# Optimization experiments

Measured on AMD Instinct MI355X. Metric: run time of the kernel, lower is better.

The kernel has to match this reference:

```python
import jax, jax.numpy as jnp
import numpy as np

B, N, D = 4, 1024, 32      # clouds, points per cloud, feature dim
NW = 4                     # n_weights
THRESHOLD = 0.5
J = 3                      # wavelet scales (as in forward: J = 3)


def setup_inputs() -> dict:
    key = jax.random.key(0)
    k1, k2 = jax.random.split(key)
    point_clouds = jax.random.normal(k1, (B, N, D), dtype=jnp.float32)
    alphas = jax.random.uniform(k2, (NW, D), dtype=jnp.float32)
    sigma = jnp.float32(50.0)
    return {"point_clouds": point_clouds, "alphas": alphas, "sigma": sigma}


def reference(point_clouds, alphas, sigma):
    # X_nodes = pc * alpha_w for every (cloud p, weight w): [B, NW, N, D]
    X = point_clouds[:, None, :, :] * alphas[None, :, None, :]
    # compute_dist: ||xi||^2 + ||xj||^2 - 2 <xi, xj>  -> [B, NW, N, N]
    sq = jnp.sum(X * X, axis=-1)
    G = jnp.einsum('bwnd,bwmd->bwnm', X, X)
    Dm = sq[..., :, None] + sq[..., None, :] - 2.0 * G
    K = jnp.exp(-Dm / sigma)
    # threshold graph: keep kernel weight where K >= threshold (self-loops kept, K_ii = 1)
    A = (K >= THRESHOLD).astype(X.dtype)
    Wm = K * A
    deg = jnp.sum(Wm, axis=-1)  # >= 1 via self-loop
    # lazy random-walk diffusion operator P = 0.5 (I + D^{-1} W)
    P = 0.5 * (jnp.eye(N, dtype=X.dtype) + Wm / deg[..., None])
    # dyadic powers P^(2^j), j = 0..J
    powers = [P]
    for _ in range(J):
        powers.append(jnp.einsum('bwnm,bwmk->bwnk', powers[-1], powers[-1]))

    def apply(M, F):
        return jnp.einsum('bwnm,bwmd->bwnd', M, F)

    # first-order scattering |psi_j X| with psi_j = P^(2^(j)) - P^(2^(j+1))
    first = [jnp.abs(apply(powers[j] - powers[j + 1], X)) for j in range(J)]
    # second-order |psi_k |psi_j X|| for j < k
    second = [jnp.abs(apply(powers[k] - powers[k + 1], first[j]))
              for j in range(J) for k in range(j + 1, J)]
    feats = jnp.concatenate([X] + first + second, axis=-1)  # [B, NW, N, F0]
    pooled = jnp.mean(feats, axis=2)                        # mean pooling -> [B, NW, F0]
    # final view(B_pc, features * n_weights)
    return pooled.reshape(B, -1)
```

## Files before the change

kernel.cpp:

```cpp
#include <hip/hip_runtime.h>
#include <math.h>

#define NPTS 1024
#define DIM 32
#define NPAIR 16

typedef __attribute__((ext_vector_type(8))) short short8;
typedef __attribute__((ext_vector_type(4))) float f32x4;
typedef __attribute__((ext_vector_type(8))) unsigned short ushort8v;
typedef unsigned short u16;
typedef unsigned char u8;


__device__ __forceinline__ u16 bf16_rne(float v) {
    unsigned u = __float_as_uint(v);
    return (u16)((u + 0x7fffu + ((u >> 16) & 1u)) >> 16);
}
__device__ __forceinline__ float bf16_to_f32(u16 b) {
    return __uint_as_float(((unsigned)b) << 16);
}

__device__ __forceinline__ short8 unpack_w8(unsigned lo, unsigned hi) {
    short8 r;
#pragma unroll
    for (int j = 0; j < 4; j++) {
        float f0 = (float)((lo >> (8 * j)) & 0xffu);
        float f1 = (float)((hi >> (8 * j)) & 0xffu);
        r[j]     = (short)(__float_as_uint(f0) >> 16);
        r[j + 4] = (short)(__float_as_uint(f1) >> 16);
    }
    return r;
}

__global__ __launch_bounds__(256) void build_X(const float* __restrict__ pc,
                                               const float* __restrict__ alphas,
                                               float* __restrict__ X,
                                               float* __restrict__ sqX,
                                               float* __restrict__ deg,
                                               u16* __restrict__ hiT,
                                               u16* __restrict__ loT,
                                               float* __restrict__ poolP) {
    __shared__ float S[DIM][68];
    int pair = blockIdx.y, n0 = blockIdx.x * 64, tid = threadIdx.x;
    int b = pair >> 2, w = pair & 3;
    for (int e = tid; e < 512; e += 256) {
        int e4 = e * 4;
        int dn = e4 >> 5, dq = e4 & 31;
        float4 p = *(const float4*)&pc[((size_t)b * NPTS + n0 + dn) * DIM + dq];
        float4 al = *(const float4*)&alphas[w * DIM + dq];
        float4 x = make_float4(p.x * al.x, p.y * al.y, p.z * al.z, p.w * al.w);
        *(float4*)&X[((size_t)pair * NPTS + n0 + dn) * DIM + dq] = x;
        S[dq][dn] = x.x; S[dq + 1][dn] = x.y; S[dq + 2][dn] = x.z; S[dq + 3][dn] = x.w;
    }
    __syncthreads();
    if (tid < 64) {
        float s = 0.f;
#pragma unroll
        for (int d = 0; d < DIM; d++) { float v = S[d][tid]; s += v * v; }
        sqX[pair * NPTS + n0 + tid] = s;
        deg[pair * NPTS + n0 + tid] = 0.0f;
    }
    if (tid < 64) {
        int h = tid >> 5, d = tid & 31;
        float s = 0.f;
#pragma unroll
        for (int k = 0; k < 32; k++) s += S[d][h * 32 + k];
        poolP[(((size_t)0 * NPAIR + pair) * 32 + 2 * blockIdx.x + h) * 32 + d] = s;
    }
    for (int idx = tid; idx < DIM * 4; idx += 256) {
        int row = idx >> 2, nq = (idx & 3) * 16;
        ushort8v hv[2], lv[2];
#pragma unroll
        for (int i = 0; i < 16; i++) {
            float v = S[row][nq + i];
            u16 hb = bf16_rne(v);
            hv[i >> 3][i & 7] = hb;
            lv[i >> 3][i & 7] = bf16_rne(v - bf16_to_f32(hb));
        }
        int c0 = n0 + nq;
        int kt = c0 >> 5;
        int q0 = (c0 >> 3) & 3;
        int mm = row & 15;
        size_t base = ((((size_t)pair * 2 + (row >> 4)) * 32 + kt) << 9);
        *(ushort8v*)(hiT + base + (size_t)(q0 * 16 + mm) * 8)       = hv[0];
        *(ushort8v*)(hiT + base + (size_t)((q0 + 1) * 16 + mm) * 8) = hv[1];
        *(ushort8v*)(loT + base + (size_t)(q0 * 16 + mm) * 8)       = lv[0];
        *(ushort8v*)(loT + base + (size_t)((q0 + 1) * 16 + mm) * 8) = lv[1];
    }
}

__global__ __launch_bounds__(256, 4) void W_kernel(const float* __restrict__ X,
                                                   const float* __restrict__ sqX,
                                                   const float* __restrict__ sigp,
                                                   float* __restrict__ deg,
                                                   u8* __restrict__ W8) {
    int bid = blockIdx.x;
    int xcd = bid & 7, loc = bid >> 3;
    int pair = xcd * 2 + (loc & 1);
    int j0 = ((loc >> 1) & 3) * 256;
    int i0 = (loc >> 3) * 64;
    float rsig = -1.0f / (*sigp);
    const float* Xp = X + (size_t)pair * NPTS * DIM;

    __shared__ float XiT[DIM][68];
    __shared__ float XjT[DIM][68];
    __shared__ float sqjS[64];

    int tid = threadIdx.x;
    int cx = tid & 15, ry = tid >> 4;

    {
        int r = tid & 63, dgb = (tid >> 6) * 4;
#pragma unroll
        for (int p = 0; p < 2; p++) {
            int dg = dgb + p * 16;
            float4 v = *(const float4*)&Xp[(size_t)(i0 + r) * DIM + dg];
            XiT[dg][r] = v.x; XiT[dg + 1][r] = v.y; XiT[dg + 2][r] = v.z; XiT[dg + 3][r] = v.w;
        }
    }
    float sqi[4];
#pragma unroll
    for (int a = 0; a < 4; a++) sqi[a] = sqX[pair * NPTS + i0 + ry * 4 + a];

    float rs[4] = {0.f, 0.f, 0.f, 0.f};
#pragma unroll 1
    for (int jt = 0; jt < 256; jt += 64) {
        __syncthreads();
        {
            int r = tid & 63, dgb = (tid >> 6) * 4;
#pragma unroll
            for (int p = 0; p < 2; p++) {
                int dg = dgb + p * 16;
                float4 v = *(const float4*)&Xp[(size_t)(j0 + jt + r) * DIM + dg];
                XjT[dg][r] = v.x; XjT[dg + 1][r] = v.y; XjT[dg + 2][r] = v.z; XjT[dg + 3][r] = v.w;
            }
        }
        if (tid < 64) sqjS[tid] = sqX[pair * NPTS + j0 + jt + tid];
        __syncthreads();

        float dot[4][4] = {};
#pragma unroll
        for (int d = 0; d < DIM; d++) {
            float4 a = *(const float4*)&XiT[d][ry * 4];
            float4 b = *(const float4*)&XjT[d][cx * 4];
            dot[0][0] += a.x * b.x; dot[0][1] += a.x * b.y; dot[0][2] += a.x * b.z; dot[0][3] += a.x * b.w;
            dot[1][0] += a.y * b.x; dot[1][1] += a.y * b.y; dot[1][2] += a.y * b.z; dot[1][3] += a.y * b.w;
            dot[2][0] += a.z * b.x; dot[2][1] += a.z * b.y; dot[2][2] += a.z * b.z; dot[2][3] += a.z * b.w;
            dot[3][0] += a.w * b.x; dot[3][1] += a.w * b.y; dot[3][2] += a.w * b.z; dot[3][3] += a.w * b.w;
        }
#pragma unroll
        for (int a = 0; a < 4; a++) {
            int i = i0 + ry * 4 + a;
            int jb = j0 + jt + cx * 4;
            unsigned qw = 0;
#pragma unroll
            for (int bb = 0; bb < 4; bb++) {
                float Dm = sqi[a] + sqjS[cx * 4 + bb] - 2.0f * dot[a][bb];
                float K = __expf(Dm * rsig);
                float Wv = (K >= 0.5f) ? K : 0.0f;
                unsigned q = (unsigned)fmaf(Wv, 255.0f, 0.5f);
                rs[a] += (float)q;
                qw |= q << (8 * bb);
            }
            int kt = jb >> 5;
            int quad = (jb >> 3) & 3;
            int jj = jb & 7;
            size_t o = ((((size_t)pair * 64 + (i >> 4)) * 32 + kt) << 9)
                     + (size_t)(quad * 16 + (i & 15)) * 8 + jj;
            *(unsigned*)(W8 + o) = qw;
        }
    }
#pragma unroll
    for (int a = 0; a < 4; a++) {
        float s = rs[a];
        s += __shfl_xor(s, 1); s += __shfl_xor(s, 2);
        s += __shfl_xor(s, 4); s += __shfl_xor(s, 8);
        if (cx == 0) atomicAdd(&deg[pair * NPTS + i0 + ry * 4 + a], s);
    }
}

template <int DC>
__global__ __launch_bounds__(512, 4) void apply_fused(const u8* __restrict__ W8,
                                                      const u16* __restrict__ Yhi,
                                                      const u16* __restrict__ Ylo,
                                                      const float* __restrict__ deg,
                                                      const float* __restrict__ prevF,
                                                      int prevStride, int prevOff,
                                                      float* __restrict__ dstF,
                                                      int dstStride, int dstOff,
                                                      float* __restrict__ sliceF,
                                                      u16* __restrict__ hiT, u16* __restrict__ loT,
                                                      int tC0, int tCN) {
    constexpr int NT = DC / 16;
    constexpr int SP = DC + 4;
    __shared__ float S[4][32][SP];
    __shared__ float rdegS[32];
    int bid = blockIdx.x;
    int pair = (bid & 7) * 2 + ((bid >> 3) & 1);
    int r0 = (bid >> 4) * 32;
    int tid = threadIdx.x;
    int wv = tid >> 6, lane = tid & 63;
    int m = lane & 15, quad = lane >> 4;

    if (tid < 32) rdegS[tid] = 0.5f / deg[pair * NPTS + r0 + tid];

    int rt0 = (bid >> 4) * 2;
    const u8*  Wb  = W8  + ((((size_t)pair * 64 + rt0) * 32 + wv * 4) << 9) + (size_t)lane * 8;
    const u16* Ybh = Yhi + (((size_t)pair * NT * 32 + wv * 4) << 9) + (size_t)lane * 8;
    const u16* Ybl = Ylo + (((size_t)pair * NT * 32 + wv * 4) << 9) + (size_t)lane * 8;

    f32x4 acc[2][NT];
#pragma unroll
    for (int mt = 0; mt < 2; mt++)
#pragma unroll
        for (int nt = 0; nt < NT; nt++)
#pragma unroll
            for (int i = 0; i < 4; i++) acc[mt][nt][i] = 0.0f;

#pragma unroll 2
    for (int c = 0; c < 4; c++) {
        uint2 a0q = *(const uint2*)(Wb + ((size_t)c << 9));
        uint2 a1q = *(const uint2*)(Wb + ((size_t)(32 + c) << 9));
        short8 a0h = unpack_w8(a0q.x, a0q.y);
        short8 a1h = unpack_w8(a1q.x, a1q.y);
#pragma unroll
        for (int nt = 0; nt < NT; nt++) {
            short8 bh = *(const short8*)(Ybh + ((size_t)(nt * 32 + c) << 9));
            short8 bl = *(const short8*)(Ybl + ((size_t)(nt * 32 + c) << 9));
            acc[0][nt] = __builtin_amdgcn_mfma_f32_16x16x32_bf16(a0h, bh, acc[0][nt], 0, 0, 0);
            acc[0][nt] = __builtin_amdgcn_mfma_f32_16x16x32_bf16(a0h, bl, acc[0][nt], 0, 0, 0);
            acc[1][nt] = __builtin_amdgcn_mfma_f32_16x16x32_bf16(a1h, bh, acc[1][nt], 0, 0, 0);
            acc[1][nt] = __builtin_amdgcn_mfma_f32_16x16x32_bf16(a1h, bl, acc[1][nt], 0, 0, 0);
        }
    }

    if (wv < 4) {
#pragma unroll
        for (int mt = 0; mt < 2; mt++)
#pragma unroll
            for (int nt = 0; nt < NT; nt++)
#pragma unroll
                for (int i = 0; i < 4; i++)
                    S[wv][mt * 16 + quad * 4 + i][nt * 16 + m] = acc[mt][nt][i];
    }
    __syncthreads();
    if (wv >= 4) {
#pragma unroll
        for (int mt = 0; mt < 2; mt++)
#pragma unroll
            for (int nt = 0; nt < NT; nt++)
#pragma unroll
                for (int i = 0; i < 4; i++)
                    S[wv - 4][mt * 16 + quad * 4 + i][nt * 16 + m] += acc[mt][nt][i];
    }
    __syncthreads();

    constexpr int E2 = 32 * DC / 4;
    for (int e = tid; e < E2; e += 512) {
        int e4 = e * 4;
        int n = e4 / DC, d = e4 % DC;
        float4 s0 = *(const float4*)&S[0][n][d];
        float4 s1 = *(const float4*)&S[1][n][d];
        float4 s2 = *(const float4*)&S[2][n][d];
        float4 s3 = *(const float4*)&S[3][n][d];
        float4 pv = *(const float4*)&prevF[((size_t)pair * NPTS + r0 + n) * prevStride + prevOff + d];
        float r = rdegS[n];
        float4 o = make_float4(0.5f * pv.x + r * (s0.x + s1.x + s2.x + s3.x),
                               0.5f * pv.y + r * (s0.y + s1.y + s2.y + s3.y),
                               0.5f * pv.z + r * (s0.z + s1.z + s2.z + s3.z),
                               0.5f * pv.w + r * (s0.w + s1.w + s2.w + s3.w));
        *(float4*)&dstF[((size_t)pair * NPTS + r0 + n) * dstStride + dstOff + d] = o;
        if (sliceF && d >= 32 && d < 64)
            *(float4*)&sliceF[((size_t)pair * NPTS + r0 + n) * 32 + (d - 32)] = o;
        *(float4*)&S[0][n][d] = o;
    }
    __syncthreads();

    if (hiT) {
        int NFo = tCN >> 4;
        for (int e = tid; e < tCN * 4; e += 512) {
            int row = e >> 2, nq = (e & 3) * 8;
            ushort8v hv, lv;
#pragma unroll
            for (int j = 0; j < 8; j++) {
                float v = S[0][nq + j][tC0 + row];
                u16 hb = bf16_rne(v);
                hv[j] = hb;
                lv[j] = bf16_rne(v - bf16_to_f32(hb));
            }
            int c0 = r0 + nq;
            size_t o = ((((size_t)pair * NFo + (row >> 4)) * 32 + (c0 >> 5)) << 9)
                     + (size_t)((((c0 >> 3) & 3) * 16 + (row & 15))) * 8;
            *(ushort8v*)(hiT + o) = hv;
            *(ushort8v*)(loT + o) = lv;
        }
    }
}

__global__ __launch_bounds__(512, 4) void apply_fused_m0(const u8* __restrict__ W8,
                                                         const u16* __restrict__ Yhi,
                                                         const u16* __restrict__ Ylo,
                                                         const float* __restrict__ deg,
                                                         const float* __restrict__ prevF,
                                                         const float* __restrict__ A1,
                                                         const float* __restrict__ A2,
                                                         float* __restrict__ M0,
                                                         u16* __restrict__ hiT, u16* __restrict__ loT,
                                                         float* __restrict__ poolP) {
    constexpr int DC = 32, NT = 2, SP = 36;
    __shared__ float S[4][32][SP];
    __shared__ float rdegS[32];
    __shared__ float SB[96][33];
    int bid = blockIdx.x;
    int pair = (bid & 7) * 2 + ((bid >> 3) & 1);
    int r0 = (bid >> 4) * 32;
    int rt = bid >> 4;
    int tid = threadIdx.x;
    int wv = tid >> 6, lane = tid & 63;
    int m = lane & 15, quad = lane >> 4;

    if (tid < 32) rdegS[tid] = 0.5f / deg[pair * NPTS + r0 + tid];

    int rt0 = rt * 2;
    const u8*  Wb  = W8  + ((((size_t)pair * 64 + rt0) * 32 + wv * 4) << 9) + (size_t)lane * 8;
    const u16* Ybh = Yhi + (((size_t)pair * NT * 32 + wv * 4) << 9) + (size_t)lane * 8;
    const u16* Ybl = Ylo + (((size_t)pair * NT * 32 + wv * 4) << 9) + (size_t)lane * 8;

    f32x4 acc[2][NT];
#pragma unroll
    for (int mt = 0; mt < 2; mt++)
#pragma unroll
        for (int nt = 0; nt < NT; nt++)
#pragma unroll
            for (int i = 0; i < 4; i++) acc[mt][nt][i] = 0.0f;

#pragma unroll 2
    for (int c = 0; c < 4; c++) {
        uint2 a0q = *(const uint2*)(Wb + ((size_t)c << 9));
        uint2 a1q = *(const uint2*)(Wb + ((size_t)(32 + c) << 9));
        short8 a0h = unpack_w8(a0q.x, a0q.y);
        short8 a1h = unpack_w8(a1q.x, a1q.y);
#pragma unroll
        for (int nt = 0; nt < NT; nt++) {
            short8 bh = *(const short8*)(Ybh + ((size_t)(nt * 32 + c) << 9));
            short8 bl = *(const short8*)(Ybl + ((size_t)(nt * 32 + c) << 9));
            acc[0][nt] = __builtin_amdgcn_mfma_f32_16x16x32_bf16(a0h, bh, acc[0][nt], 0, 0, 0);
            acc[0][nt] = __builtin_amdgcn_mfma_f32_16x16x32_bf16(a0h, bl, acc[0][nt], 0, 0, 0);
            acc[1][nt] = __builtin_amdgcn_mfma_f32_16x16x32_bf16(a1h, bh, acc[1][nt], 0, 0, 0);
            acc[1][nt] = __builtin_amdgcn_mfma_f32_16x16x32_bf16(a1h, bl, acc[1][nt], 0, 0, 0);
        }
    }

    if (wv < 4) {
#pragma unroll
        for (int mt = 0; mt < 2; mt++)
#pragma unroll
            for (int nt = 0; nt < NT; nt++)
#pragma unroll
                for (int i = 0; i < 4; i++)
                    S[wv][mt * 16 + quad * 4 + i][nt * 16 + m] = acc[mt][nt][i];
    }
    __syncthreads();
    if (wv >= 4) {
#pragma unroll
        for (int mt = 0; mt < 2; mt++)
#pragma unroll
            for (int nt = 0; nt < NT; nt++)
#pragma unroll
                for (int i = 0; i < 4; i++)
                    S[wv - 4][mt * 16 + quad * 4 + i][nt * 16 + m] += acc[mt][nt][i];
    }
    __syncthreads();

    for (int e = tid; e < 256; e += 512) {
        int e4 = e * 4;
        int n = e4 / DC, d = e4 % DC;
        float4 s0 = *(const float4*)&S[0][n][d];
        float4 s1 = *(const float4*)&S[1][n][d];
        float4 s2 = *(const float4*)&S[2][n][d];
        float4 s3 = *(const float4*)&S[3][n][d];
        float4 pv = *(const float4*)&prevF[((size_t)pair * NPTS + r0 + n) * 32 + d];
        float r = rdegS[n];
        float4 o = make_float4(0.5f * pv.x + r * (s0.x + s1.x + s2.x + s3.x),
                               0.5f * pv.y + r * (s0.y + s1.y + s2.y + s3.y),
                               0.5f * pv.z + r * (s0.z + s1.z + s2.z + s3.z),
                               0.5f * pv.w + r * (s0.w + s1.w + s2.w + s3.w));
        *(float4*)&M0[((size_t)pair * NPTS + r0 + n) * 96 + d] = o;
        *(float4*)&S[0][n][d] = o;
    }
    __syncthreads();

    if (tid < 256) {
        int dn = tid >> 3, dq = (tid & 7) * 4;
        size_t pn = (size_t)pair * NPTS + r0 + dn;
        float4 a1 = *(const float4*)&A1[pn * 32 + dq];
        float4 a2 = *(const float4*)&A2[pn * 32 + dq];
        float4 t4 = *(const float4*)&S[0][dn][dq];
        float4 f0 = make_float4(fabsf(a1.x - a2.x), fabsf(a1.y - a2.y), fabsf(a1.z - a2.z), fabsf(a1.w - a2.w));
        float4 f1 = make_float4(fabsf(a2.x - t4.x), fabsf(a2.y - t4.y), fabsf(a2.z - t4.z), fabsf(a2.w - t4.w));
        *(float4*)&M0[pn * 96 + 32 + dq] = f0;
        *(float4*)&M0[pn * 96 + 64 + dq] = f1;
        SB[dq][dn] = t4.x; SB[dq + 1][dn] = t4.y; SB[dq + 2][dn] = t4.z; SB[dq + 3][dn] = t4.w;
        SB[32 + dq][dn] = f0.x; SB[33 + dq][dn] = f0.y; SB[34 + dq][dn] = f0.z; SB[35 + dq][dn] = f0.w;
        SB[64 + dq][dn] = f1.x; SB[65 + dq][dn] = f1.y; SB[66 + dq][dn] = f1.z; SB[67 + dq][dn] = f1.w;
    }
    __syncthreads();

    if (tid < 64) {
        int gg = tid >> 5, d = tid & 31;
        float s = 0.f;
#pragma unroll
        for (int k = 0; k < 32; k++) s += SB[32 + gg * 32 + d][k];
        poolP[(((size_t)(1 + gg) * NPAIR + pair) * 32 + rt) * 32 + d] = s;
    }

    for (int e = tid; e < 96 * 4; e += 512) {
        int row = e >> 2, nq = (e & 3) * 8;
        ushort8v hv, lv;
#pragma unroll
        for (int j = 0; j < 8; j++) {
            float v = SB[row][nq + j];
            u16 hb = bf16_rne(v);
            hv[j] = hb;
            lv[j] = bf16_rne(v - bf16_to_f32(hb));
        }
        int c0 = r0 + nq;
        size_t o = ((((size_t)pair * 6 + (row >> 4)) * 32 + (c0 >> 5)) << 9)
                 + (size_t)((((c0 >> 3) & 3) * 16 + (row & 15))) * 8;
        *(ushort8v*)(hiT + o) = hv;
        *(ushort8v*)(loT + o) = lv;
    }
}

__global__ __launch_bounds__(512, 4) void apply_fused_pool(const u8* __restrict__ W8,
                                                           const u16* __restrict__ Yhi,
                                                           const u16* __restrict__ Ylo,
                                                           const float* __restrict__ deg,
                                                           const float* __restrict__ prevF,
                                                           float* __restrict__ Z8,
                                                           const float* __restrict__ M0,
                                                           const float* __restrict__ M2p,
                                                           const float* __restrict__ M4f,
                                                           float* __restrict__ poolP) {
    constexpr int DC = 64, NT = 4, SP = 68;
    __shared__ float S[4][32][SP];
    __shared__ float rdegS[32];
    __shared__ float PP[4][2][32];
    int bid = blockIdx.x;
    int pair = (bid & 7) * 2 + ((bid >> 3) & 1);
    int r0 = (bid >> 4) * 32;
    int rt = bid >> 4;
    int tid = threadIdx.x;
    int wv = tid >> 6, lane = tid & 63;
    int m = lane & 15, quad = lane >> 4;

    if (tid < 32) rdegS[tid] = 0.5f / deg[pair * NPTS + r0 + tid];

    int rt0 = rt * 2;
    const u8*  Wb  = W8  + ((((size_t)pair * 64 + rt0) * 32 + wv * 4) << 9) + (size_t)lane * 8;
    const u16* Ybh = Yhi + (((size_t)pair * NT * 32 + wv * 4) << 9) + (size_t)lane * 8;
    const u16* Ybl = Ylo + (((size_t)pair * NT * 32 + wv * 4) << 9) + (size_t)lane * 8;

    f32x4 acc[2][NT];
#pragma unroll
    for (int mt = 0; mt < 2; mt++)
#pragma unroll
        for (int nt = 0; nt < NT; nt++)
#pragma unroll
            for (int i = 0; i < 4; i++) acc[mt][nt][i] = 0.0f;

#pragma unroll 2
    for (int c = 0; c < 4; c++) {
        uint2 a0q = *(const uint2*)(Wb + ((size_t)c << 9));
        uint2 a1q = *(const uint2*)(Wb + ((size_t)(32 + c) << 9));
        short8 a0h = unpack_w8(a0q.x, a0q.y);
        short8 a1h = unpack_w8(a1q.x, a1q.y);
#pragma unroll
        for (int nt = 0; nt < NT; nt++) {
            short8 bh = *(const short8*)(Ybh + ((size_t)(nt * 32 + c) << 9));
            short8 bl = *(const short8*)(Ybl + ((size_t)(nt * 32 + c) << 9));
            acc[0][nt] = __builtin_amdgcn_mfma_f32_16x16x32_bf16(a0h, bh, acc[0][nt], 0, 0, 0);
            acc[0][nt] = __builtin_amdgcn_mfma_f32_16x16x32_bf16(a0h, bl, acc[0][nt], 0, 0, 0);
            acc[1][nt] = __builtin_amdgcn_mfma_f32_16x16x32_bf16(a1h, bh, acc[1][nt], 0, 0, 0);
            acc[1][nt] = __builtin_amdgcn_mfma_f32_16x16x32_bf16(a1h, bl, acc[1][nt], 0, 0, 0);
        }
    }

    if (wv < 4) {
#pragma unroll
        for (int mt = 0; mt < 2; mt++)
#pragma unroll
            for (int nt = 0; nt < NT; nt++)
#pragma unroll
                for (int i = 0; i < 4; i++)
                    S[wv][mt * 16 + quad * 4 + i][nt * 16 + m] = acc[mt][nt][i];
    }
    __syncthreads();
    if (wv >= 4) {
#pragma unroll
        for (int mt = 0; mt < 2; mt++)
#pragma unroll
            for (int nt = 0; nt < NT; nt++)
#pragma unroll
                for (int i = 0; i < 4; i++)
                    S[wv - 4][mt * 16 + quad * 4 + i][nt * 16 + m] += acc[mt][nt][i];
    }
    __syncthreads();

    for (int e = tid; e < 512; e += 512) {
        int e4 = e * 4;
        int n = e4 / DC, d = e4 % DC;
        float4 s0 = *(const float4*)&S[0][n][d];
        float4 s1 = *(const float4*)&S[1][n][d];
        float4 s2 = *(const float4*)&S[2][n][d];
        float4 s3 = *(const float4*)&S[3][n][d];
        float4 pv = *(const float4*)&prevF[((size_t)pair * NPTS + r0 + n) * 64 + d];
        float r = rdegS[n];
        float4 o = make_float4(0.5f * pv.x + r * (s0.x + s1.x + s2.x + s3.x),
                               0.5f * pv.y + r * (s0.y + s1.y + s2.y + s3.y),
                               0.5f * pv.z + r * (s0.z + s1.z + s2.z + s3.z),
                               0.5f * pv.w + r * (s0.w + s1.w + s2.w + s3.w));
        *(float4*)&Z8[((size_t)pair * NPTS + r0 + n) * 64 + d] = o;
        *(float4*)&S[0][n][d] = o;
    }
    __syncthreads();

    if (tid < 256) {
        int gsel = tid >> 6, h = (tid >> 5) & 1, d = tid & 31;
        float s = 0.f;
#pragma unroll 4
        for (int k = 0; k < 16; k++) {
            int n = h * 16 + k;
            size_t pn = (size_t)pair * NPTS + r0 + n;
            float v;
            switch (gsel) {
                case 0: v = fabsf(M0[pn * 96 + d] - M4f[pn * 96 + d]); break;
                case 1: v = fabsf(M2p[pn * 32 + d] - M4f[pn * 96 + 32 + d]); break;
                case 2: v = fabsf(M4f[pn * 96 + 32 + d] - S[0][n][d]); break;
                default: v = fabsf(M4f[pn * 96 + 64 + d] - S[0][n][32 + d]); break;
            }
            s += v;
        }
        PP[gsel][h][d] = s;
    }
    __syncthreads();
    if (tid < 128) {
        int gsel = tid >> 5, d = tid & 31;
        poolP[(((size_t)(3 + gsel) * NPAIR + pair) * 32 + rt) * 32 + d] = PP[gsel][0][d] + PP[gsel][1][d];
    }
}

__global__ __launch_bounds__(256) void pool_final(const float* __restrict__ partial,
                                                  float* __restrict__ out) {
    int pair = blockIdx.x;
    int t = threadIdx.x;
    if (t < 224) {
        int g = t >> 5, d = t & 31;
        float s = 0.0f;
#pragma unroll 8
        for (int r = 0; r < 32; r++)
            s += partial[(((size_t)g * NPAIR + pair) * 32 + r) * 32 + d];
        out[(size_t)pair * 224 + t] = s * (1.0f / 1024.0f);
    }
}

extern "C" void kernel_launch(void* const* d_in, const int* in_sizes, int n_in,
                              void* d_out, int out_size, void* d_ws, size_t ws_size,
                              hipStream_t stream) {
    const float* pc     = (const float*)d_in[0];
    const float* alphas = (const float*)d_in[1];
    const float* sigp   = (const float*)d_in[2];
    float* out = (float*)d_out;
    float* ws = (float*)d_ws;

    float* X    = ws;
    float* sqX  = X + 524288;
    float* deg  = sqX + 16384;
    u8* W8 = (u8*)(deg + 16384);
    float* A1   = (float*)(W8 + 16777216);
    float* A2   = A1 + 524288;
    u16* T32a_h = (u16*)(A2 + 524288);
    u16* T32a_l = T32a_h + 524288;
    u16* T32b_h = T32a_l + 524288;
    u16* T32b_l = T32b_h + 524288;
    float* F96b = A1;
    float* M0   = (float*)(T32b_l + 524288);
    float* M2p  = M0 + 1572864;
    float* M4f  = M2p + 524288;
    float* Z8   = M4f + 1572864;
    float* F96a = Z8 + 1048576;
    float* A3   = F96a;
    u16* T96a_h = (u16*)(F96a + 1572864);
    u16* T96a_l = T96a_h + 1572864;
    u16* T96b_h = T96a_l + 1572864;
    u16* T96b_l = T96b_h + 1572864;
    u16* T64a_h = T96a_h;
    u16* T64a_l = T96a_l;
    u16* T64b_h = T96b_h;
    u16* T64b_l = T96b_l;
    float* poolP = (float*)(T96b_l + 1572864);

    dim3 b256(256), b512(512);

    build_X<<<dim3(16, NPAIR), b256, 0, stream>>>(pc, alphas, X, sqX, deg, T32a_h, T32a_l, poolP);
    W_kernel<<<dim3(1024), b256, 0, stream>>>(X, sqX, sigp, deg, W8);

    apply_fused<32><<<dim3(512), b512, 0, stream>>>(W8, T32a_h, T32a_l, deg,
                                             X, 32, 0, A1, 32, 0, nullptr, T32b_h, T32b_l, 0, 32);
    apply_fused<32><<<dim3(512), b512, 0, stream>>>(W8, T32b_h, T32b_l, deg,
                                             A1, 32, 0, A2, 32, 0, nullptr, T32a_h, T32a_l, 0, 32);
    apply_fused<32><<<dim3(512), b512, 0, stream>>>(W8, T32a_h, T32a_l, deg,
                                             A2, 32, 0, A3, 32, 0, nullptr, T32b_h, T32b_l, 0, 32);
    apply_fused_m0<<<dim3(512), b512, 0, stream>>>(W8, T32b_h, T32b_l, deg,
                                             A3, A1, A2, M0, T96a_h, T96a_l, poolP);

    apply_fused<96><<<dim3(512), b512, 0, stream>>>(W8, T96a_h, T96a_l, deg,
                                             M0, 96, 0, F96a, 96, 0, nullptr, T96b_h, T96b_l, 0, 96);
    apply_fused<96><<<dim3(512), b512, 0, stream>>>(W8, T96b_h, T96b_l, deg,
                                             F96a, 96, 0, F96b, 96, 0, M2p, T96a_h, T96a_l, 0, 96);
    apply_fused<96><<<dim3(512), b512, 0, stream>>>(W8, T96a_h, T96a_l, deg,
                                             F96b, 96, 0, F96a, 96, 0, nullptr, T96b_h, T96b_l, 0, 96);
    apply_fused<96><<<dim3(512), b512, 0, stream>>>(W8, T96b_h, T96b_l, deg,
                                             F96a, 96, 0, M4f, 96, 0, nullptr, T64a_h, T64a_l, 32, 64);

    apply_fused<64><<<dim3(512), b512, 0, stream>>>(W8, T64a_h, T64a_l, deg,
                                             M4f, 96, 32, F96a, 64, 0, nullptr, T64b_h, T64b_l, 0, 64);
    apply_fused<64><<<dim3(512), b512, 0, stream>>>(W8, T64b_h, T64b_l, deg,
                                             F96a, 64, 0, F96b, 64, 0, nullptr, T64a_h, T64a_l, 0, 64);
    apply_fused<64><<<dim3(512), b512, 0, stream>>>(W8, T64a_h, T64a_l, deg,
                                             F96b, 64, 0, F96a, 64, 0, nullptr, T64b_h, T64b_l, 0, 64);
    apply_fused_pool<<<dim3(512), b512, 0, stream>>>(W8, T64b_h, T64b_l, deg,
                                             F96a, Z8, M0, M2p, M4f, poolP);

    pool_final<<<dim3(NPAIR), b256, 0, stream>>>(poolP, out);
}
```

Before: 235.2 us.

## Retile wide apply kernels to 64-row by 32-column blocks split over column chunks

Adds apply_fused2 and apply_fused_pool2, which give each block 64 rows and one 32-column chunk of the feature matrix instead of 32 rows and all columns. The 96- and 64-column diffusion applies and the final pooling kernel now use this tiling, with more blocks for the 96-wide case. Each loaded W tile is reused across four row tiles per wave and the number of resident accumulators per thread is bounded. In exchange, the W8 matrix is re-read once per column chunk, and the pooling partial sums are split by chunk with direct writes to poolP.

Result: faster. 224.5 us (-4.6%).

```diff
diff --git a/kernel.cpp b/kernel.cpp
--- a/kernel.cpp
+++ b/kernel.cpp
@@ -297,6 +297,130 @@
     }
 }
 
+template <int DC>
+__global__ __launch_bounds__(512, 4) void apply_fused2(const u8* __restrict__ W8,
+                                                       const u16* __restrict__ Yhi,
+                                                       const u16* __restrict__ Ylo,
+                                                       const float* __restrict__ deg,
+                                                       const float* __restrict__ prevF,
+                                                       int prevStride, int prevOff,
+                                                       float* __restrict__ dstF,
+                                                       int dstStride, int dstOff,
+                                                       float* __restrict__ sliceF,
+                                                       u16* __restrict__ hiT, u16* __restrict__ loT,
+                                                       int tC0, int tCN) {
+    constexpr int NF = DC / 16;
+    constexpr int SP = 36;
+    __shared__ float S[4][64][SP];
+    __shared__ float rdegS[64];
+    int bid = blockIdx.x;
+    int pair = (bid & 7) * 2 + ((bid >> 3) & 1);
+    int rseg = (bid >> 4) & 15;
+    int ch = bid >> 8;
+    int r0 = rseg * 64;
+    int tid = threadIdx.x;
+    int wv = tid >> 6, lane = tid & 63;
+    int m = lane & 15, quad = lane >> 4;
+
+    if (tid < 64) rdegS[tid] = 0.5f / deg[pair * NPTS + r0 + tid];
+
+    const u8*  Wb  = W8  + ((((size_t)pair * 64 + rseg * 4) * 32 + wv * 4) << 9) + (size_t)lane * 8;
+    const u16* Ybh = Yhi + ((((size_t)pair * NF + ch * 2) * 32 + wv * 4) << 9) + (size_t)lane * 8;
+    const u16* Ybl = Ylo + ((((size_t)pair * NF + ch * 2) * 32 + wv * 4) << 9) + (size_t)lane * 8;
+
+    f32x4 acc[4][2];
+#pragma unroll
+    for (int mt = 0; mt < 4; mt++)
+#pragma unroll
+        for (int nt = 0; nt < 2; nt++)
+#pragma unroll
+            for (int i = 0; i < 4; i++) acc[mt][nt][i] = 0.0f;
+
+#pragma unroll 2
+    for (int c = 0; c < 4; c++) {
+        uint2 aq[4];
+#pragma unroll
+        for (int mt = 0; mt < 4; mt++)
+            aq[mt] = *(const uint2*)(Wb + ((size_t)(mt * 32 + c) << 9));
+        short8 a[4];
+#pragma unroll
+        for (int mt = 0; mt < 4; mt++) a[mt] = unpack_w8(aq[mt].x, aq[mt].y);
+#pragma unroll
+        for (int nt = 0; nt < 2; nt++) {
+            short8 bh = *(const short8*)(Ybh + ((size_t)(nt * 32 + c) << 9));
+            short8 bl = *(const short8*)(Ybl + ((size_t)(nt * 32 + c) << 9));
+#pragma unroll
+            for (int mt = 0; mt < 4; mt++) {
+                acc[mt][nt] = __builtin_amdgcn_mfma_f32_16x16x32_bf16(a[mt], bh, acc[mt][nt], 0, 0, 0);
+                acc[mt][nt] = __builtin_amdgcn_mfma_f32_16x16x32_bf16(a[mt], bl, acc[mt][nt], 0, 0, 0);
+            }
+        }
+    }
+
+    if (wv < 4) {
+#pragma unroll
+        for (int mt = 0; mt < 4; mt++)
+#pragma unroll
+            for (int nt = 0; nt < 2; nt++)
+#pragma unroll
+                for (int i = 0; i < 4; i++)
+                    S[wv][mt * 16 + quad * 4 + i][nt * 16 + m] = acc[mt][nt][i];
+    }
+    __syncthreads();
+    if (wv >= 4) {
+#pragma unroll
+        for (int mt = 0; mt < 4; mt++)
+#pragma unroll
+            for (int nt = 0; nt < 2; nt++)
+#pragma unroll
+                for (int i = 0; i < 4; i++)
+                    S[wv - 4][mt * 16 + quad * 4 + i][nt * 16 + m] += acc[mt][nt][i];
+    }
+    __syncthreads();
+
+    {
+        int n = tid >> 3, d = (tid & 7) * 4;
+        int col = ch * 32 + d;
+        float4 s0 = *(const float4*)&S[0][n][d];
+        float4 s1 = *(const float4*)&S[1][n][d];
+        float4 s2 = *(const float4*)&S[2][n][d];
+        float4 s3 = *(const float4*)&S[3][n][d];
+        float4 pv = *(const float4*)&prevF[((size_t)pair * NPTS + r0 + n) * prevStride + prevOff + col];
+        float r = rdegS[n];
+        float4 o = make_float4(0.5f * pv.x + r * (s0.x + s1.x + s2.x + s3.x),
+                               0.5f * pv.y + r * (s0.y + s1.y + s2.y + s3.y),
+                               0.5f * pv.z + r * (s0.z + s1.z + s2.z + s3.z),
+                               0.5f * pv.w + r * (s0.w + s1.w + s2.w + s3.w));
+        *(float4*)&dstF[((size_t)pair * NPTS + r0 + n) * dstStride + dstOff + col] = o;
+        if (sliceF && ch == 1)
+            *(float4*)&sliceF[((size_t)pair * NPTS + r0 + n) * 32 + d] = o;
+        *(float4*)&S[0][n][d] = o;
+    }
+    __syncthreads();
+
+    int gr0 = 32 * ch - tC0;
+    if (hiT && gr0 >= 0 && gr0 < tCN) {
+        int NFo = tCN >> 4;
+        if (tid < 256) {
+            int lr = tid >> 3, nq = (tid & 7) * 8;
+            ushort8v hv, lv;
+#pragma unroll
+            for (int j = 0; j < 8; j++) {
+                float v = S[0][nq + j][lr];
+                u16 hb = bf16_rne(v);
+                hv[j] = hb;
+                lv[j] = bf16_rne(v - bf16_to_f32(hb));
+            }
+            int gr = gr0 + lr;
+            int c0 = r0 + nq;
+            size_t o = ((((size_t)pair * NFo + (gr >> 4)) * 32 + (c0 >> 5)) << 9)
+                     + (size_t)((((c0 >> 3) & 3) * 16 + (gr & 15))) * 8;
+            *(ushort8v*)(hiT + o) = hv;
+            *(ushort8v*)(loT + o) = lv;
+        }
+    }
+}
+
 __global__ __launch_bounds__(512, 4) void apply_fused_m0(const u8* __restrict__ W8,
                                                          const u16* __restrict__ Yhi,
                                                          const u16* __restrict__ Ylo,
@@ -432,65 +556,68 @@
     }
 }
 
-__global__ __launch_bounds__(512, 4) void apply_fused_pool(const u8* __restrict__ W8,
-                                                           const u16* __restrict__ Yhi,
-                                                           const u16* __restrict__ Ylo,
-                                                           const float* __restrict__ deg,
-                                                           const float* __restrict__ prevF,
-                                                           float* __restrict__ Z8,
-                                                           const float* __restrict__ M0,
-                                                           const float* __restrict__ M2p,
-                                                           const float* __restrict__ M4f,
-                                                           float* __restrict__ poolP) {
-    constexpr int DC = 64, NT = 4, SP = 68;
-    __shared__ float S[4][32][SP];
-    __shared__ float rdegS[32];
-    __shared__ float PP[4][2][32];
+__global__ __launch_bounds__(512, 4) void apply_fused_pool2(const u8* __restrict__ W8,
+                                                            const u16* __restrict__ Yhi,
+                                                            const u16* __restrict__ Ylo,
+                                                            const float* __restrict__ deg,
+                                                            const float* __restrict__ prevF,
+                                                            float* __restrict__ Z8,
+                                                            const float* __restrict__ M0,
+                                                            const float* __restrict__ M2p,
+                                                            const float* __restrict__ M4f,
+                                                            float* __restrict__ poolP) {
+    constexpr int NF = 4, SP = 36;
+    __shared__ float S[4][64][SP];
+    __shared__ float rdegS[64];
     int bid = blockIdx.x;
     int pair = (bid & 7) * 2 + ((bid >> 3) & 1);
-    int r0 = (bid >> 4) * 32;
-    int rt = bid >> 4;
+    int rseg = (bid >> 4) & 15;
+    int ch = bid >> 8;
+    int r0 = rseg * 64;
     int tid = threadIdx.x;
     int wv = tid >> 6, lane = tid & 63;
     int m = lane & 15, quad = lane >> 4;
 
-    if (tid < 32) rdegS[tid] = 0.5f / deg[pair * NPTS + r0 + tid];
-
-    int rt0 = rt * 2;
-    const u8*  Wb  = W8  + ((((size_t)pair * 64 + rt0) * 32 + wv * 4) << 9) + (size_t)lane * 8;
-    const u16* Ybh = Yhi + (((size_t)pair * NT * 32 + wv * 4) << 9) + (size_t)lane * 8;
-    const u16* Ybl = Ylo + (((size_t)pair * NT * 32 + wv * 4) << 9) + (size_t)lane * 8;
-
-    f32x4 acc[2][NT];
-#pragma unroll
-    for (int mt = 0; mt < 2; mt++)
-#pragma unroll
-        for (int nt = 0; nt < NT; nt++)
+    if (tid < 64) rdegS[tid] = 0.5f / deg[pair * NPTS + r0 + tid];
+
+    const u8*  Wb  = W8  + ((((size_t)pair * 64 + rseg * 4) * 32 + wv * 4) << 9) + (size_t)lane * 8;
+    const u16* Ybh = Yhi + ((((size_t)pair * NF + ch * 2) * 32 + wv * 4) << 9) + (size_t)lane * 8;
+    const u16* Ybl = Ylo + ((((size_t)pair * NF + ch * 2) * 32 + wv * 4) << 9) + (size_t)lane * 8;
+
+    f32x4 acc[4][2];
+#pragma unroll
+    for (int mt = 0; mt < 4; mt++)
+#pragma unroll
+        for (int nt = 0; nt < 2; nt++)
 #pragma unroll
             for (int i = 0; i < 4; i++) acc[mt][nt][i] = 0.0f;
 
 #pragma unroll 2
     for (int c = 0; c < 4; c++) {
-        uint2 a0q = *(const uint2*)(Wb + ((size_t)c << 9));
-        uint2 a1q = *(const uint2*)(Wb + ((size_t)(32 + c) << 9));
-        short8 a0h = unpack_w8(a0q.x, a0q.y);
-        short8 a1h = unpack_w8(a1q.x, a1q.y);
-#pragma unroll
-        for (int nt = 0; nt < NT; nt++) {
+        uint2 aq[4];
+#pragma unroll
+        for (int mt = 0; mt < 4; mt++)
+            aq[mt] = *(const uint2*)(Wb + ((size_t)(mt * 32 + c) << 9));
+        short8 a[4];
+#pragma unroll
+        for (int mt = 0; mt < 4; mt++) a[mt] = unpack_w8(aq[mt].x, aq[mt].y);
+#pragma unroll
+        for (int nt = 0; nt < 2; nt++) {
             short8 bh = *(const short8*)(Ybh + ((size_t)(nt * 32 + c) << 9));
             short8 bl = *(const short8*)(Ybl + ((size_t)(nt * 32 + c) << 9));
-            acc[0][nt] = __builtin_amdgcn_mfma_f32_16x16x32_bf16(a0h, bh, acc[0][nt], 0, 0, 0);
-            acc[0][nt] = __builtin_amdgcn_mfma_f32_16x16x32_bf16(a0h, bl, acc[0][nt], 0, 0, 0);
-            acc[1][nt] = __builtin_amdgcn_mfma_f32_16x16x32_bf16(a1h, bh, acc[1][nt], 0, 0, 0);
-            acc[1][nt] = __builtin_amdgcn_mfma_f32_16x16x32_bf16(a1h, bl, acc[1][nt], 0, 0, 0);
+#pragma unroll
+            for (int mt = 0; mt < 4; mt++) {
+                acc[mt][nt] = __builtin_amdgcn_mfma_f32_16x16x32_bf16(a[mt], bh, acc[mt][nt], 0, 0, 0);
+                acc[mt][nt] = __builtin_amdgcn_mfma_f32_16x16x32_bf16(a[mt], bl, acc[mt][nt], 0, 0, 0);
+            }
         }
     }
 
     if (wv < 4) {
 #pragma unroll
-        for (int mt = 0; mt < 2; mt++)
-#pragma unroll
-            for (int nt = 0; nt < NT; nt++)
+        for (int mt = 0; mt < 4; mt++)
+#pragma unroll
+            for (int nt = 0; nt < 2; nt++)
 #pragma unroll
                 for (int i = 0; i < 4; i++)
                     S[wv][mt * 16 + quad * 4 + i][nt * 16 + m] = acc[mt][nt][i];
@@ -498,55 +625,63 @@
     __syncthreads();
     if (wv >= 4) {
 #pragma unroll
-        for (int mt = 0; mt < 2; mt++)
-#pragma unroll
-            for (int nt = 0; nt < NT; nt++)
+        for (int mt = 0; mt < 4; mt++)
+#pragma unroll
+            for (int nt = 0; nt < 2; nt++)
 #pragma unroll
                 for (int i = 0; i < 4; i++)
                     S[wv - 4][mt * 16 + quad * 4 + i][nt * 16 + m] += acc[mt][nt][i];
     }
     __syncthreads();
 
-    for (int e = tid; e < 512; e += 512) {
-        int e4 = e * 4;
-        int n = e4 / DC, d = e4 % DC;
+    {
+        int n = tid >> 3, d = (tid & 7) * 4;
+        int col = ch * 32 + d;
         float4 s0 = *(const float4*)&S[0][n][d];
         float4 s1 = *(const float4*)&S[1][n][d];
         float4 s2 = *(const float4*)&S[2][n][d];
         float4 s3 = *(const float4*)&S[3][n][d];
-        float4 pv = *(const float4*)&prevF[((size_t)pair * NPTS + r0 + n) * 64 + d];
+        float4 pv = *(const float4*)&prevF[((size_t)pair * NPTS + r0 + n) * 64 + col];
         float r = rdegS[n];
         float4 o = make_float4(0.5f * pv.x + r * (s0.x + s1.x + s2.x + s3.x),
                                0.5f * pv.y + r * (s0.y + s1.y + s2.y + s3.y),
                                0.5f * pv.z + r * (s0.z + s1.z + s2.z + s3.z),
                                0.5f * pv.w + r * (s0.w + s1.w + s2.w + s3.w));
-        *(float4*)&Z8[((size_t)pair * NPTS + r0 + n) * 64 + d] = o;
+        *(float4*)&Z8[((size_t)pair * NPTS + r0 + n) * 64 + col] = o;
         *(float4*)&S[0][n][d] = o;
     }
     __syncthreads();
 
-    if (tid < 256) {
-        int gsel = tid >> 6, h = (tid >> 5) & 1, d = tid & 31;
-        float s = 0.f;
+    if (ch == 0) {
+        if (tid < 192) {
+            int gsel = tid >> 6, h = (tid >> 5) & 1, d = tid & 31;
+            float s = 0.f;
 #pragma unroll 4
-        for (int k = 0; k < 16; k++) {
-            int n = h * 16 + k;
-            size_t pn = (size_t)pair * NPTS + r0 + n;
-            float v;
-            switch (gsel) {
-                case 0: v = fabsf(M0[pn * 96 + d] - M4f[pn * 96 + d]); break;
-                case 1: v = fabsf(M2p[pn * 32 + d] - M4f[pn * 96 + 32 + d]); break;
-                case 2: v = fabsf(M4f[pn * 96 + 32 + d] - S[0][n][d]); break;
-                default: v = fabsf(M4f[pn * 96 + 64 + d] - S[0][n][32 + d]); break;
+            for (int k = 0; k < 32; k++) {
+                int n = h * 32 + k;
+                size_t pn = (size_t)pair * NPTS + r0 + n;
+                float v;
+                switch (gsel) {
+                    case 0: v = fabsf(M0[pn * 96 + d] - M4f[pn * 96 + d]); break;
+                    case 1: v = fabsf(M2p[pn * 32 + d] - M4f[pn * 96 + 32 + d]); break;
+                    default: v = fabsf(M4f[pn * 96 + 32 + d] - S[0][n][d]); break;
+                }
+                s += v;
             }
-            s += v;
-        }
-        PP[gsel][h][d] = s;
-    }
-    __syncthreads();
-    if (tid < 128) {
-        int gsel = tid >> 5, d = tid & 31;
-        poolP[(((size_t)(3 + gsel) * NPAIR + pair) * 32 + rt) * 32 + d] = PP[gsel][0][d] + PP[gsel][1][d];
+            poolP[(((size_t)(3 + gsel) * NPAIR + pair) * 32 + 2 * rseg + h) * 32 + d] = s;
+        }
+    } else {
+        if (tid < 64) {
+            int h = tid >> 5, d = tid & 31;
+            float s = 0.f;
+#pragma unroll 4
+            for (int k = 0; k < 32; k++) {
+                int n = h * 32 + k;
+                size_t pn = (size_t)pair * NPTS + r0 + n;
+                s += fabsf(M4f[pn * 96 + 64 + d] - S[0][n][d]);
+            }
+            poolP[(((size_t)6 * NPAIR + pair) * 32 + 2 * rseg + h) * 32 + d] = s;
+        }
     }
 }
 
@@ -614,22 +749,22 @@
     apply_fused_m0<<<dim3(512), b512, 0, stream>>>(W8, T32b_h, T32b_l, deg,
                                              A3, A1, A2, M0, T96a_h, T96a_l, poolP);
 
-    apply_fused<96><<<dim3(512), b512, 0, stream>>>(W8, T96a_h, T96a_l, deg,
+    apply_fused2<96><<<dim3(768), b512, 0, stream>>>(W8, T96a_h, T96a_l, deg,
                                              M0, 96, 0, F96a, 96, 0, nullptr, T96b_h, T96b_l, 0, 96);
-    apply_fused<96><<<dim3(512), b512, 0, stream>>>(W8, T96b_h, T96b_l, deg,
+    apply_fused2<96><<<dim3(768), b512, 0, stream>>>(W8, T96b_h, T96b_l, deg,
                                              F96a, 96, 0, F96b, 96, 0, M2p, T96a_h, T96a_l, 0, 96);
-    apply_fused<96><<<dim3(512), b512, 0, stream>>>(W8, T96a_h, T96a_l, deg,
+    apply_fused2<96><<<dim3(768), b512, 0, stream>>>(W8, T96a_h, T96a_l, deg,
                                              F96b, 96, 0, F96a, 96, 0, nullptr, T96b_h, T96b_l, 0, 96);
-    apply_fused<96><<<dim3(512), b512, 0, stream>>>(W8, T96b_h, T96b_l, deg,
+    apply_fused2<96><<<dim3(768), b512, 0, stream>>>(W8, T96b_h, T96b_l, deg,
                                              F96a, 96, 0, M4f, 96, 0, nullptr, T64a_h, T64a_l, 32, 64);
 
-    apply_fused<64><<<dim3(512), b512, 0, stream>>>(W8, T64a_h, T64a_l, deg,
+    apply_fused2<64><<<dim3(512), b512, 0, stream>>>(W8, T64a_h, T64a_l, deg,
                                              M4f, 96, 32, F96a, 64, 0, nullptr, T64b_h, T64b_l, 0, 64);
-    apply_fused<64><<<dim3(512), b512, 0, stream>>>(W8, T64b_h, T64b_l, deg,
+    apply_fused2<64><<<dim3(512), b512, 0, stream>>>(W8, T64b_h, T64b_l, deg,
                                              F96a, 64, 0, F96b, 64, 0, nullptr, T64a_h, T64a_l, 0, 64);
-    apply_fused<64><<<dim3(512), b512, 0, stream>>>(W8, T64a_h, T64a_l, deg,
+    apply_fused2<64><<<dim3(512), b512, 0, stream>>>(W8, T64a_h, T64a_l, deg,
                                              F96b, 64, 0, F96a, 64, 0, nullptr, T64b_h, T64b_l, 0, 64);
-    apply_fused_pool<<<dim3(512), b512, 0, stream>>>(W8, T64b_h, T64b_l, deg,
+    apply_fused_pool2<<<dim3(512), b512, 0, stream>>>(W8, T64b_h, T64b_l, deg,
                                              F96a, Z8, M0, M2p, M4f, poolP);
 
     pool_final<<<dim3(NPAIR), b256, 0, stream>>>(poolP, out);
```
